# Kernel tuning notes

Measured on AMD Instinct MI355X. Metric: run time of the kernel, lower is better.

Reference implementation:

```python
import jax, jax.numpy as jnp
import numpy as np

B = 65536      # batch of (state, action) pairs
DIM_S = 64     # input feature dim
DIM_C = 8      # number of options / experts
H = 256        # hidden width (two hidden layers)


def setup_inputs() -> dict:
    key = jax.random.key(0)
    ks = jax.random.split(key, 7)
    s = 0.05  # small init scale
    st = jax.random.normal(ks[0], (B, DIM_S), dtype=jnp.float32)
    # Batched expert weights: one slice per expert (dim_c experts).
    W1 = jax.random.normal(ks[1], (DIM_C, DIM_S, H), dtype=jnp.float32) * s
    b1 = jax.random.normal(ks[2], (DIM_C, H), dtype=jnp.float32) * s
    W2 = jax.random.normal(ks[3], (DIM_C, H, H), dtype=jnp.float32) * s
    b2 = jax.random.normal(ks[4], (DIM_C, H), dtype=jnp.float32) * s
    W3 = jax.random.normal(ks[5], (DIM_C, H, 1), dtype=jnp.float32) * s
    b3 = jax.random.normal(ks[6], (DIM_C, 1), dtype=jnp.float32) * s
    return {"st": st, "W1": W1, "b1": b1, "W2": W2, "b2": b2,
            "W3": W3, "b3": b3}


def reference(st, W1, b1, W2, b2, W3, b3):
    # Equivalent of torch.stack([m(st) for m in self.discriminator], dim=1):
    # every expert MLP (dim_s -> H -> H -> 1, ReLU) applied to the same st,
    # expressed as batched GEMMs over the expert axis c.
    h = jax.nn.relu(jnp.einsum('bs,csh->bch', st, W1) + b1[None])   # [B, C, H]
    h = jax.nn.relu(jnp.einsum('bch,chk->bck', h, W2) + b2[None])   # [B, C, H]
    d = jnp.einsum('bch,cho->bco', h, W3) + b3[None]                # [B, C, 1]
    return d
```

## Files before the change

### kernel.cpp

```cpp
#include <hip/hip_runtime.h>
#include <hip/hip_bf16.h>

typedef __bf16 bf16x8 __attribute__((ext_vector_type(8)));
typedef float  f32x4  __attribute__((ext_vector_type(4)));

static constexpr int S  = 64;
static constexpr int C  = 8;
static constexpr int HD = 256;

__device__ __forceinline__ unsigned short f2bf(float f) {
  __hip_bfloat16 b = __float2bfloat16(f);
  unsigned short u;
  __builtin_memcpy(&u, &b, 2);
  return u;
}

__device__ __forceinline__ void gl2lds16(const void* g, void* l) {
  __builtin_amdgcn_global_load_lds(
      (const __attribute__((address_space(1))) unsigned int*)g,
      (__attribute__((address_space(3))) unsigned int*)l, 16, 0, 0);
}

__global__ __launch_bounds__(256) void prep_weights(
    const float* __restrict__ W1, const float* __restrict__ W2,
    unsigned short* __restrict__ W1T, unsigned short* __restrict__ W2T)
{
  __shared__ float tile[32][33];
  const int tid = threadIdx.x, cl = tid & 31, r0 = tid >> 5;
  const int b = blockIdx.x;
  if (b < 512) {
    const int c = b >> 6, t = b & 63, kt = t >> 3, nt = t & 7;
    const float* src = W2 + c * 65536;
    #pragma unroll
    for (int i = 0; i < 4; ++i) {
      int r = r0 + 8 * i;
      tile[r][cl] = src[(kt * 32 + r) * 256 + nt * 32 + cl];
    }
    __syncthreads();
    unsigned short* dst = W2T + c * 65536;
    #pragma unroll
    for (int i = 0; i < 4; ++i) {
      int r = r0 + 8 * i;
      dst[(nt * 32 + r) * 256 + kt * 32 + cl] = f2bf(tile[cl][r]);
    }
  } else {
    const int bb = b - 512;
    const int c = bb >> 4, t = bb & 15, st2 = t >> 3, ht = t & 7;
    const float* src = W1 + c * 16384;
    #pragma unroll
    for (int i = 0; i < 4; ++i) {
      int r = r0 + 8 * i;
      tile[r][cl] = src[(st2 * 32 + r) * 256 + ht * 32 + cl];
    }
    __syncthreads();
    unsigned short* dst = W1T + c * 16384;
    #pragma unroll
    for (int i = 0; i < 4; ++i) {
      int r = r0 + 8 * i;
      dst[(ht * 32 + r) * 64 + st2 * 32 + cl] = f2bf(tile[cl][r]);
    }
  }
}

__global__ __launch_bounds__(256, 2) void moe_fused(
    const float* __restrict__ st,
    const unsigned short* __restrict__ W1T,
    const unsigned short* __restrict__ W2T,
    const float* __restrict__ b1,
    const float* __restrict__ b2,
    const float* __restrict__ W3,
    const float* __restrict__ b3,
    float* __restrict__ out)
{
  constexpr int LDT = 72;

  __shared__ __align__(16) unsigned short sT[256 * LDT];
  __shared__ __align__(16) unsigned short sU[2 * 32 * 256];

  const int tid  = threadIdx.x;
  const int lane = tid & 63;
  const int wv   = tid >> 6;
  const int l15  = lane & 15;
  const int q    = lane >> 4;
  const int c    = blockIdx.x >> 8;
  const int row0 = (blockIdx.x & 255) * 256;
  const int wrow = row0 + wv * 64;

  const unsigned short* W1c = W1T + c * HD * S;
  const unsigned short* W2c = W2T + c * HD * HD;

  float4 sraw[8][2];
  #pragma unroll
  for (int nt = 0; nt < 4; ++nt)
    #pragma unroll
    for (int ks = 0; ks < 2; ++ks) {
      const float* rp = st + (size_t)(wrow + nt * 16 + l15) * S + ks * 32 + q * 8;
      sraw[ks * 4 + nt][0] = *reinterpret_cast<const float4*>(rp);
      sraw[ks * 4 + nt][1] = *reinterpret_cast<const float4*>(rp + 4);
    }

  #pragma unroll
  for (int pc = 0; pc < 2; ++pc) {
    unsigned short* buf = sU + pc * (32 * 256);
    #pragma unroll
    for (int i = 0; i < 4; ++i) {
      const int b2i = wv * 4 + i;
      const int r   = b2i * 2 + (lane >> 5);
      const int j   = (lane & 31) ^ (r & 7);
      gl2lds16(W2c + (pc * 32 + r) * 256 + j * 8, buf + b2i * 512);
    }
  }

  bf16x8 bB[2][4];
  #pragma unroll
  for (int nt = 0; nt < 4; ++nt)
    #pragma unroll
    for (int ks = 0; ks < 2; ++ks) {
      float4 x = sraw[ks * 4 + nt][0], y = sraw[ks * 4 + nt][1];
      union { bf16x8 v; unsigned u[4]; } pk;
      __asm__("v_cvt_pk_bf16_f32 %0, %1, %2" : "=v"(pk.u[0]) : "v"(x.x), "v"(x.y));
      __asm__("v_cvt_pk_bf16_f32 %0, %1, %2" : "=v"(pk.u[1]) : "v"(x.z), "v"(x.w));
      __asm__("v_cvt_pk_bf16_f32 %0, %1, %2" : "=v"(pk.u[2]) : "v"(y.x), "v"(y.y));
      __asm__("v_cvt_pk_bf16_f32 %0, %1, %2" : "=v"(pk.u[3]) : "v"(y.z), "v"(y.w));
      bB[ks][nt] = pk.v;
    }

  bf16x8 aF[4][4][2];
  #pragma unroll
  for (int cc = 0; cc < 4; ++cc) {
    f32x4 bias[4];
    #pragma unroll
    for (int mt = 0; mt < 4; ++mt)
      bias[mt] = *reinterpret_cast<const f32x4*>(
          b1 + c * HD + cc * 64 + mt * 16 + q * 4);

    f32x4 acc[4][4];
    #pragma unroll
    for (int mt = 0; mt < 4; ++mt)
      #pragma unroll
      for (int nt = 0; nt < 4; ++nt)
        acc[mt][nt] = bias[mt];

    #pragma unroll
    for (int ks = 0; ks < 2; ++ks) {
      bf16x8 aW[4];
      #pragma unroll
      for (int mt = 0; mt < 4; ++mt)
        aW[mt] = *reinterpret_cast<const bf16x8*>(
            W1c + (cc * 64 + mt * 16 + l15) * S + ks * 32 + q * 8);
      __builtin_amdgcn_s_setprio(1);
      #pragma unroll
      for (int mt = 0; mt < 4; ++mt)
        #pragma unroll
        for (int nt = 0; nt < 4; ++nt)
          acc[mt][nt] = __builtin_amdgcn_mfma_f32_16x16x32_bf16(
              aW[mt], bB[ks][nt], acc[mt][nt], 0, 0, 0);
      __builtin_amdgcn_s_setprio(0);
    }

    #pragma unroll
    for (int mt = 0; mt < 4; ++mt) {
      #pragma unroll
      for (int nt = 0; nt < 4; ++nt) {
        float v0 = acc[mt][nt][0]; v0 = v0 > 0.f ? v0 : 0.f;
        float v1 = acc[mt][nt][1]; v1 = v1 > 0.f ? v1 : 0.f;
        float v2 = acc[mt][nt][2]; v2 = v2 > 0.f ? v2 : 0.f;
        float v3 = acc[mt][nt][3]; v3 = v3 > 0.f ? v3 : 0.f;
        uint2 pk;
        __asm__("v_cvt_pk_bf16_f32 %0, %1, %2" : "=v"(pk.x) : "v"(v0), "v"(v1));
        __asm__("v_cvt_pk_bf16_f32 %0, %1, %2" : "=v"(pk.y) : "v"(v2), "v"(v3));
        *reinterpret_cast<uint2*>(
            sT + (wv * 64 + nt * 16 + l15) * LDT + mt * 16 + q * 4) = pk;
      }
    }
    __asm__ __volatile__("s_waitcnt lgkmcnt(0)" ::: "memory");
    #pragma unroll
    for (int rt = 0; rt < 4; ++rt)
      #pragma unroll
      for (int k2 = 0; k2 < 2; ++k2)
        aF[cc][rt][k2] = *reinterpret_cast<const bf16x8*>(
            sT + (wv * 64 + rt * 16 + l15) * LDT + k2 * 32 + q * 8);
    __asm__ __volatile__("s_waitcnt lgkmcnt(0)" ::: "memory");
  }

  float pb2v[8][2], pw3v[8][2];
  #pragma unroll
  for (int ch = 0; ch < 8; ++ch)
    #pragma unroll
    for (int ct = 0; ct < 2; ++ct) {
      const int n = ch * 32 + ct * 16 + l15;
      pb2v[ch][ct] = b2[c * HD + n];
      pw3v[ch][ct] = W3[c * HD + n];
    }
  const float bb3 = b3[c];

  __syncthreads();

  float dacc[4][4];
  #pragma unroll
  for (int rt = 0; rt < 4; ++rt)
    #pragma unroll
    for (int r = 0; r < 4; ++r) dacc[rt][r] = 0.f;

  #pragma unroll
  for (int ch = 0; ch < 8; ++ch) {
    const unsigned short* buf = sU + (ch & 1) * (32 * 256);

    f32x4 acc[4][2];
    #pragma unroll
    for (int rt = 0; rt < 4; ++rt)
      #pragma unroll
      for (int ct = 0; ct < 2; ++ct) {
        const float bv = pb2v[ch][ct];
        acc[rt][ct] = (f32x4){bv, bv, bv, bv};
      }

    #pragma unroll
    for (int ks = 0; ks < 8; ++ks) {
      const int jj = ks * 4 + q;
      const int cc = ks >> 1, k2 = ks & 1;
      #pragma unroll
      for (int ct = 0; ct < 2; ++ct) {
        const int nl = ct * 16 + l15;
        bf16x8 b = *reinterpret_cast<const bf16x8*>(
            buf + nl * 256 + ((jj ^ (l15 & 7)) << 3));
        __builtin_amdgcn_s_setprio(1);
        #pragma unroll
        for (int rt = 0; rt < 4; ++rt)
          acc[rt][ct] = __builtin_amdgcn_mfma_f32_16x16x32_bf16(
              aF[cc][rt][k2], b, acc[rt][ct], 0, 0, 0);
        __builtin_amdgcn_s_setprio(0);
      }
    }

    #pragma unroll
    for (int ct = 0; ct < 2; ++ct) {
      const float w3v = pw3v[ch][ct];
      #pragma unroll
      for (int rt = 0; rt < 4; ++rt)
        #pragma unroll
        for (int r = 0; r < 4; ++r) {
          float v = acc[rt][ct][r];
          v = v > 0.f ? v : 0.f;
          dacc[rt][r] += v * w3v;
        }
    }

    __syncthreads();
    if (ch < 6) {
      unsigned short* nbuf = sU + (ch & 1) * (32 * 256);
      #pragma unroll
      for (int i = 0; i < 4; ++i) {
        const int b2i = wv * 4 + i;
        const int r   = b2i * 2 + (lane >> 5);
        const int j   = (lane & 31) ^ (r & 7);
        gl2lds16(W2c + ((ch + 2) * 32 + r) * 256 + j * 8, nbuf + b2i * 512);
      }
    }
  }

  #pragma unroll
  for (int rt = 0; rt < 4; ++rt)
    #pragma unroll
    for (int r = 0; r < 4; ++r) {
      float v = dacc[rt][r];
      v += __shfl_xor(v, 1);
      v += __shfl_xor(v, 2);
      v += __shfl_xor(v, 4);
      v += __shfl_xor(v, 8);
      dacc[rt][r] = v;
    }

  if (l15 == 0) {
    const int rbase = row0 + wv * 64 + q * 4;
    #pragma unroll
    for (int rt = 0; rt < 4; ++rt)
      #pragma unroll
      for (int r = 0; r < 4; ++r)
        out[(rbase + rt * 16 + r) * C + c] = dacc[rt][r] + bb3;
  }
}

extern "C" void kernel_launch(void* const* d_in, const int* in_sizes, int n_in,
                              void* d_out, int out_size, void* d_ws, size_t ws_size,
                              hipStream_t stream)
{
  const float* st = (const float*)d_in[0];
  const float* W1 = (const float*)d_in[1];
  const float* b1 = (const float*)d_in[2];
  const float* W2 = (const float*)d_in[3];
  const float* b2 = (const float*)d_in[4];
  const float* W3 = (const float*)d_in[5];
  const float* b3 = (const float*)d_in[6];
  float* out = (float*)d_out;

  unsigned short* W1T = (unsigned short*)d_ws;
  unsigned short* W2T = W1T + C * HD * S;

  prep_weights<<<dim3(640), dim3(256), 0, stream>>>(W1, W2, W1T, W2T);
  moe_fused<<<dim3(2048), dim3(256), 0, stream>>>(st, W1T, W2T, b1, b2, W3, b3, out);
}
```

Baseline: 172.3 us.

## Transpose layer-1 activations in registers via permlane swaps; double W2 staging chunks

Replaces the LDS round-trip that turned layer-1 MFMA outputs into layer-2 A-operand fragments with an in-register transpose built from v_permlane32/16_swap, and removes the sT buffer. The freed shared memory goes to a larger W2 staging area: four 32-row chunks are prefetched, and the pipeline now syncs once per pair of chunks instead of once per chunk. This is meant to cut LDS write/read traffic, lgkm waits, and barrier count. The risk is that the register fragment layout produced by the lane swaps must exactly match the old LDS layout, and that register pressure rises.

New measurement: 165.5 us. -3.9%, faster.

```diff
diff --git a/kernel.cpp b/kernel.cpp
--- a/kernel.cpp
+++ b/kernel.cpp
@@ -72,10 +72,7 @@
     const float* __restrict__ b3,
     float* __restrict__ out)
 {
-  constexpr int LDT = 72;
-
-  __shared__ __align__(16) unsigned short sT[256 * LDT];
-  __shared__ __align__(16) unsigned short sU[2 * 32 * 256];
+  __shared__ __align__(16) unsigned short sU[4 * 32 * 256];
 
   const int tid  = threadIdx.x;
   const int lane = tid & 63;
@@ -100,14 +97,14 @@
     }
 
   #pragma unroll
-  for (int pc = 0; pc < 2; ++pc) {
-    unsigned short* buf = sU + pc * (32 * 256);
+  for (int ck = 0; ck < 4; ++ck) {
+    unsigned short* buf = sU + ck * 8192;
     #pragma unroll
     for (int i = 0; i < 4; ++i) {
       const int b2i = wv * 4 + i;
       const int r   = b2i * 2 + (lane >> 5);
       const int j   = (lane & 31) ^ (r & 7);
-      gl2lds16(W2c + (pc * 32 + r) * 256 + j * 8, buf + b2i * 512);
+      gl2lds16(W2c + (ck * 32 + r) * 256 + j * 8, buf + b2i * 512);
     }
   }
 
@@ -159,28 +156,32 @@
     }
 
     #pragma unroll
-    for (int mt = 0; mt < 4; ++mt) {
-      #pragma unroll
-      for (int nt = 0; nt < 4; ++nt) {
-        float v0 = acc[mt][nt][0]; v0 = v0 > 0.f ? v0 : 0.f;
-        float v1 = acc[mt][nt][1]; v1 = v1 > 0.f ? v1 : 0.f;
-        float v2 = acc[mt][nt][2]; v2 = v2 > 0.f ? v2 : 0.f;
-        float v3 = acc[mt][nt][3]; v3 = v3 > 0.f ? v3 : 0.f;
-        uint2 pk;
-        __asm__("v_cvt_pk_bf16_f32 %0, %1, %2" : "=v"(pk.x) : "v"(v0), "v"(v1));
-        __asm__("v_cvt_pk_bf16_f32 %0, %1, %2" : "=v"(pk.y) : "v"(v2), "v"(v3));
-        *reinterpret_cast<uint2*>(
-            sT + (wv * 64 + nt * 16 + l15) * LDT + mt * 16 + q * 4) = pk;
+    for (int nt = 0; nt < 4; ++nt) {
+      #pragma unroll
+      for (int k2 = 0; k2 < 2; ++k2) {
+        const f32x4& E = acc[2 * k2][nt];
+        const f32x4& O = acc[2 * k2 + 1][nt];
+        float e0 = E[0] > 0.f ? E[0] : 0.f, e1 = E[1] > 0.f ? E[1] : 0.f;
+        float e2 = E[2] > 0.f ? E[2] : 0.f, e3 = E[3] > 0.f ? E[3] : 0.f;
+        float o0 = O[0] > 0.f ? O[0] : 0.f, o1 = O[1] > 0.f ? O[1] : 0.f;
+        float o2 = O[2] > 0.f ? O[2] : 0.f, o3 = O[3] > 0.f ? O[3] : 0.f;
+        unsigned dE0, dE1, dO0, dO1;
+        __asm__("v_cvt_pk_bf16_f32 %0, %1, %2" : "=v"(dE0) : "v"(e0), "v"(e1));
+        __asm__("v_cvt_pk_bf16_f32 %0, %1, %2" : "=v"(dE1) : "v"(e2), "v"(e3));
+        __asm__("v_cvt_pk_bf16_f32 %0, %1, %2" : "=v"(dO0) : "v"(o0), "v"(o1));
+        __asm__("v_cvt_pk_bf16_f32 %0, %1, %2" : "=v"(dO1) : "v"(o2), "v"(o3));
+        __asm__("v_permlane32_swap_b32 %0, %1" : "+v"(dE0), "+v"(dO0));
+        __asm__("v_permlane16_swap_b32 %0, %1" : "+v"(dE0), "+v"(dO0));
+        __asm__("v_permlane32_swap_b32 %0, %1" : "+v"(dE1), "+v"(dO1));
+        __asm__("v_permlane16_swap_b32 %0, %1" : "+v"(dE1), "+v"(dO1));
+        union { unsigned u[4]; bf16x8 v; } f;
+        f.u[0] = dE0;
+        f.u[1] = dE1;
+        f.u[2] = dO0;
+        f.u[3] = dO1;
+        aF[cc][nt][k2] = f.v;
       }
     }
-    __asm__ __volatile__("s_waitcnt lgkmcnt(0)" ::: "memory");
-    #pragma unroll
-    for (int rt = 0; rt < 4; ++rt)
-      #pragma unroll
-      for (int k2 = 0; k2 < 2; ++k2)
-        aF[cc][rt][k2] = *reinterpret_cast<const bf16x8*>(
-            sT + (wv * 64 + rt * 16 + l15) * LDT + k2 * 32 + q * 8);
-    __asm__ __volatile__("s_waitcnt lgkmcnt(0)" ::: "memory");
   }
 
   float pb2v[8][2], pw3v[8][2];
@@ -203,58 +204,67 @@
     for (int r = 0; r < 4; ++r) dacc[rt][r] = 0.f;
 
   #pragma unroll
-  for (int ch = 0; ch < 8; ++ch) {
-    const unsigned short* buf = sU + (ch & 1) * (32 * 256);
-
-    f32x4 acc[4][2];
-    #pragma unroll
-    for (int rt = 0; rt < 4; ++rt)
+  for (int pg = 0; pg < 4; ++pg) {
+    const int bsel = pg & 1;
+    #pragma unroll
+    for (int sub = 0; sub < 2; ++sub) {
+      const int ch = 2 * pg + sub;
+      const unsigned short* buf = sU + bsel * 16384 + sub * 8192;
+
+      f32x4 acc[4][2];
+      #pragma unroll
+      for (int rt = 0; rt < 4; ++rt)
+        #pragma unroll
+        for (int ct = 0; ct < 2; ++ct) {
+          const float bv = pb2v[ch][ct];
+          acc[rt][ct] = (f32x4){bv, bv, bv, bv};
+        }
+
+      #pragma unroll
+      for (int ks = 0; ks < 8; ++ks) {
+        const int jj = ks * 4 + q;
+        const int cc = ks >> 1, k2 = ks & 1;
+        #pragma unroll
+        for (int ct = 0; ct < 2; ++ct) {
+          const int nl = ct * 16 + l15;
+          bf16x8 b = *reinterpret_cast<const bf16x8*>(
+              buf + nl * 256 + ((jj ^ (l15 & 7)) << 3));
+          __builtin_amdgcn_s_setprio(1);
+          #pragma unroll
+          for (int rt = 0; rt < 4; ++rt)
+            acc[rt][ct] = __builtin_amdgcn_mfma_f32_16x16x32_bf16(
+                aF[cc][rt][k2], b, acc[rt][ct], 0, 0, 0);
+          __builtin_amdgcn_s_setprio(0);
+        }
+      }
+
       #pragma unroll
       for (int ct = 0; ct < 2; ++ct) {
-        const float bv = pb2v[ch][ct];
-        acc[rt][ct] = (f32x4){bv, bv, bv, bv};
+        const float w3v = pw3v[ch][ct];
+        #pragma unroll
+        for (int rt = 0; rt < 4; ++rt)
+          #pragma unroll
+          for (int r = 0; r < 4; ++r) {
+            float v = acc[rt][ct][r];
+            v = v > 0.f ? v : 0.f;
+            dacc[rt][r] += v * w3v;
+          }
       }
-
-    #pragma unroll
-    for (int ks = 0; ks < 8; ++ks) {
-      const int jj = ks * 4 + q;
-      const int cc = ks >> 1, k2 = ks & 1;
-      #pragma unroll
-      for (int ct = 0; ct < 2; ++ct) {
-        const int nl = ct * 16 + l15;
-        bf16x8 b = *reinterpret_cast<const bf16x8*>(
-            buf + nl * 256 + ((jj ^ (l15 & 7)) << 3));
-        __builtin_amdgcn_s_setprio(1);
-        #pragma unroll
-        for (int rt = 0; rt < 4; ++rt)
-          acc[rt][ct] = __builtin_amdgcn_mfma_f32_16x16x32_bf16(
-              aF[cc][rt][k2], b, acc[rt][ct], 0, 0, 0);
-        __builtin_amdgcn_s_setprio(0);
-      }
-    }
-
-    #pragma unroll
-    for (int ct = 0; ct < 2; ++ct) {
-      const float w3v = pw3v[ch][ct];
-      #pragma unroll
-      for (int rt = 0; rt < 4; ++rt)
-        #pragma unroll
-        for (int r = 0; r < 4; ++r) {
-          float v = acc[rt][ct][r];
-          v = v > 0.f ? v : 0.f;
-          dacc[rt][r] += v * w3v;
+    }
+
+    __syncthreads();
+    if (pg < 2) {
+      #pragma unroll
+      for (int sub = 0; sub < 2; ++sub) {
+        unsigned short* nbuf = sU + bsel * 16384 + sub * 8192;
+        const int ch = 2 * pg + 4 + sub;
+        #pragma unroll
+        for (int i = 0; i < 4; ++i) {
+          const int b2i = wv * 4 + i;
+          const int r   = b2i * 2 + (lane >> 5);
+          const int j   = (lane & 31) ^ (r & 7);
+          gl2lds16(W2c + (ch * 32 + r) * 256 + j * 8, nbuf + b2i * 512);
         }
-    }
-
-    __syncthreads();
-    if (ch < 6) {
-      unsigned short* nbuf = sU + (ch & 1) * (32 * 256);
-      #pragma unroll
-      for (int i = 0; i < 4; ++i) {
-        const int b2i = wv * 4 + i;
-        const int r   = b2i * 2 + (lane >> 5);
-        const int j   = (lane & 31) ^ (r & 7);
-        gl2lds16(W2c + ((ch + 2) * 32 + r) * 256 + j * 8, nbuf + b2i * 512);
       }
     }
   }
```
